# Optimization experiments

Hardware: AMD Instinct MI355X
Metric: run time of the kernel (lower is better)

## Reference

```python
import jax, jax.numpy as jnp
import numpy as np

B, T, C, NH = 4, 827, 1024, 16
HS = C // NH
SCALE = 1.0 / float(np.sqrt(HS))


def setup_inputs() -> dict:
    key = jax.random.key(0)
    ks = jax.random.split(key, 16)
    d = {}
    d["x"] = jax.random.normal(ks[0], (B, T, C), jnp.float32)
    d["x_kv"] = jax.random.normal(ks[1], (B, T, C), jnp.float32)
    d["h"] = jax.random.normal(ks[2], (B, NH, T, T), jnp.float32) * 0.1
    for i, name in enumerate(["f01", "f02", "f12", "b01", "b02", "b12"]):
        d[name] = jax.random.uniform(ks[3 + i], (B, 256, 256), jnp.float32)
    for i, name in enumerate(["Wq", "Wk", "Wv", "Wp"]):
        d[name] = jax.random.normal(ks[9 + i], (C, C), jnp.float32) * 0.02
    for name in ["bq", "bk", "bv", "bp"]:
        d[name] = jnp.zeros((C,), jnp.float32)
    return d


def _sm(a):
    return jax.nn.softmax(a, axis=-1)


def reference(x, x_kv, h, f01, f02, f12, b01, b02, b12,
              Wq, bq, Wk, bk, Wv, bv, Wp, bp):
    Bb, Tt, Cc = x.shape

    def heads(t):  # [B,T,C] -> [B,NH,T,HS]
        return t.reshape(Bb, Tt, NH, HS).transpose(0, 2, 1, 3)

    q = heads(x @ Wq.T + bq)
    k = heads(x_kv @ Wk.T + bk)
    v = heads(x_kv @ Wv.T + bv)

    att = jnp.einsum('bhqd,bhkd->bhqk', q, k) * SCALE + h  # adaptive bias add

    # region-specific partial softmax (frame1->frame0, frame2->frame0, frame2->frame1)
    att = att.at[:, :, 285:541, 0:256].set(_sm(att[:, :, 285:541, 0:256]))
    att = att.at[:, :, 571:827, 0:256].set(_sm(att[:, :, 571:827, 0:256]))
    att = att.at[:, :, 571:827, 286:542].set(_sm(att[:, :, 571:827, 286:542]))

    # bidirectional epipolar maps (backward maps used transposed)
    b01t = b01.transpose(0, 2, 1)
    b02t = b02.transpose(0, 2, 1)
    b12t = b12.transpose(0, 2, 1)
    m12 = (f12 * b12t >= 0.1).astype(att.dtype)  # [B,256,256]

    # bi_epi_ratio (T==827 branch), computed BEFORE the multiplicative masking
    r3 = att[:, :, 571:827, 286:542]            # [B,NH,256,256]
    att_mean = r3.mean(-1)                       # [B,NH,256]
    att_mask_mean = (r3 * m12[:, None]).sum(-1) / m12.sum(-1)[:, None]
    bi_epi_ratio = att_mask_mean.mean(1) / att_mean.mean(1)  # [B,256]

    # att_for: forward-only masking (clone); att: forward*backward masking
    att_for = att
    att_for = att_for.at[:, :, 285:541, 0:256].multiply(f01[:, None])
    att_for = att_for.at[:, :, 571:827, 0:256].multiply(f02[:, None])
    att_for = att_for.at[:, :, 571:827, 286:542].multiply(f12[:, None])
    att = att.at[:, :, 285:541, 0:256].multiply((b01t * f01)[:, None])
    att = att.at[:, :, 571:827, 0:256].multiply((b02t * f02)[:, None])
    att = att.at[:, :, 571:827, 286:542].multiply((b12t * f12)[:, None])

    causal = jnp.tril(jnp.ones((Tt, Tt), dtype=bool))
    aw = jnp.where(causal, att, -jnp.inf)
    # re-softmax of the already masked+multiplied regions (overwrites, then global softmax)
    aw = aw.at[:, :, 571:827, 0:256].set(_sm(att[:, :, 571:827, 0:256]))
    aw = aw.at[:, :, 571:827, 286:542].set(_sm(att[:, :, 571:827, 286:542]))
    aw = _sm(aw)

    y = jnp.einsum('bhqk,bhkd->bhqd', aw, v)
    y = y.transpose(0, 2, 1, 3).reshape(Bb, Tt, Cc)
    y = y @ Wp.T + bp  # resid dropout is identity (pdrop=0 / eval)
    return y, bi_epi_ratio
```

## Files before the change

### kernel.cpp

```cpp
#include <hip/hip_runtime.h>
#include <cstdint>
#include <cstddef>

#define Tn  827
#define Cn  1024
#define BTn 3308
#define TPn 832
#define YSZ 3387392

typedef unsigned short u16;
typedef unsigned short u16x4 __attribute__((ext_vector_type(4)));
typedef __bf16 bf16_t;
typedef bf16_t bf16x8 __attribute__((ext_vector_type(8)));
typedef float f32x4 __attribute__((ext_vector_type(4)));

__device__ inline u16 f32_to_bf16(float f) {
  union { float f; unsigned u; } v; v.f = f;
  unsigned u = v.u;
  u += 0x7fffu + ((u >> 16) & 1u);
  return (u16)(u >> 16);
}

__global__ __launch_bounds__(256)
void cvt_all_k(const float* __restrict__ x, const float* __restrict__ xkv,
               const float* __restrict__ wq, const float* __restrict__ wk,
               const float* __restrict__ wv, const float* __restrict__ wp,
               u16* __restrict__ xb, u16* __restrict__ xkb,
               u16* __restrict__ wqb, u16* __restrict__ wkb,
               u16* __restrict__ wvb, u16* __restrict__ wpb)
{
  const long NX = 846848;
  const long NW = 262144;
  long qidx = (long)blockIdx.x * 256 + threadIdx.x;
  const float* s; u16* d; long base;
  if (qidx < NX)            { s = x;   d = xb;  base = qidx; }
  else if (qidx < 2 * NX)   { s = xkv; d = xkb; base = qidx - NX; }
  else {
    long w = qidx - 2 * NX;
    int wi = (int)(w / NW);
    base = w - (long)wi * NW;
    if      (wi == 0) { s = wq; d = wqb; }
    else if (wi == 1) { s = wk; d = wkb; }
    else if (wi == 2) { s = wv; d = wvb; }
    else if (wi == 3) { s = wp; d = wpb; }
    else return;
  }
  const float4 v = *(const float4*)(s + base * 4);
  u16x4 o;
  o.x = f32_to_bf16(v.x); o.y = f32_to_bf16(v.y);
  o.z = f32_to_bf16(v.z); o.w = f32_to_bf16(v.w);
  *(u16x4*)(d + base * 4) = o;
}

template<int BM, int BN, int MODE>
__global__ __launch_bounds__(256)
void gemm_k(const u16* __restrict__ Aall, const u16* __restrict__ Ball,
            const float* __restrict__ bias, float* __restrict__ Cf,
            u16* __restrict__ Cb, int M, int N, int K, int lda, int ldb, int ldc)
{
  static_assert(BM == 128, "BM fixed at 128");
  constexpr int TM = BM / 32;
  constexpr int TN = BN / 32;

  const int tid  = threadIdx.x;
  const int lane = tid & 63;
  const int wave = tid >> 6;
  const int wm = wave >> 1, wn = wave & 1;
  const int m0 = blockIdx.x * BM;
  const int n0 = blockIdx.y * BN;

  __shared__ u16 As[BM * 32];
  __shared__ u16 Bs[BN * 32];

  f32x4 acc[TM][TN];
  const f32x4 zero4 = {0.f, 0.f, 0.f, 0.f};
  #pragma unroll
  for (int i = 0; i < TM; ++i)
    #pragma unroll
    for (int j = 0; j < TN; ++j)
      acc[i][j] = zero4;

  const int nk = K >> 5;

  for (int kt = 0; kt < nk; ++kt) {
    const int k0 = kt << 5;
    __syncthreads();
    #pragma unroll
    for (int it = 0; it < BM / 64; ++it) {
      const int cbase = it * 256 + wave * 64;
      const int c  = cbase + lane;
      const int r  = c >> 2;
      const int ko = (c & 3) << 3;
      if (m0 + r < M)
        __builtin_amdgcn_global_load_lds(
            (__attribute__((address_space(1))) void*)(Aall + (size_t)(m0 + r) * lda + k0 + ko),
            (__attribute__((address_space(3))) void*)(As + cbase * 8),
            16, 0, 0);
    }
    #pragma unroll
    for (int it = 0; it < BN / 64; ++it) {
      const int cbase = it * 256 + wave * 64;
      const int c  = cbase + lane;
      const int r  = c >> 2;
      const int ko = (c & 3) << 3;
      if (n0 + r < N)
        __builtin_amdgcn_global_load_lds(
            (__attribute__((address_space(1))) void*)(Ball + (size_t)(n0 + r) * ldb + k0 + ko),
            (__attribute__((address_space(3))) void*)(Bs + cbase * 8),
            16, 0, 0);
    }
    __syncthreads();

    bf16x8 af[TM], bfr[TN];
    #pragma unroll
    for (int i = 0; i < TM; ++i) {
      const int r = wm * 64 + i * 16 + (lane & 15);
      af[i] = *(const bf16x8*)(As + r * 32 + ((lane >> 4) << 3));
    }
    #pragma unroll
    for (int j = 0; j < TN; ++j) {
      const int r = wn * (TN * 16) + j * 16 + (lane & 15);
      bfr[j] = *(const bf16x8*)(Bs + r * 32 + ((lane >> 4) << 3));
    }
    #pragma unroll
    for (int i = 0; i < TM; ++i)
      #pragma unroll
      for (int j = 0; j < TN; ++j)
        acc[i][j] = __builtin_amdgcn_mfma_f32_16x16x32_bf16(af[i], bfr[j], acc[i][j], 0, 0, 0);
  }

  const int cq = lane >> 4, cl = lane & 15;
  #pragma unroll
  for (int i = 0; i < TM; ++i) {
    #pragma unroll
    for (int j = 0; j < TN; ++j) {
      const int rb  = m0 + wm * 64 + i * 16 + cq * 4;
      const int col = n0 + wn * (TN * 16) + j * 16 + cl;
      #pragma unroll
      for (int r = 0; r < 4; ++r) {
        const int row = rb + r;
        const float v = acc[i][j][r];
        if constexpr (MODE == 0) {
          if (row < M) Cb[(size_t)row * ldc + col] = f32_to_bf16(v + bias[col]);
        } else {
          if (row < M) Cf[(size_t)row * ldc + col] = v + bias[col];
        }
      }
    }
  }
}

__global__ __launch_bounds__(256)
void vtrans_k(const u16* __restrict__ V, u16* __restrict__ Vt)
{
  const int z = blockIdx.y;
  const int b = z >> 4, hh = z & 15;
  const int k0 = blockIdx.x * 64;
  const int tid = threadIdx.x;
  __shared__ u16 tile[64 * 65];
  #pragma unroll
  for (int rep = 0; rep < 16; ++rep) {
    const int idx = rep * 256 + tid;
    const int kl = idx >> 6, n = idx & 63;
    const int k = k0 + kl;
    u16 val = 0;
    if (k < Tn) val = V[((size_t)(b * Tn + k)) * Cn + hh * 64 + n];
    tile[n * 65 + kl] = val;
  }
  __syncthreads();
  #pragma unroll
  for (int rep = 0; rep < 16; ++rep) {
    const int idx = rep * 256 + tid;
    const int n = idx >> 6, kl = idx & 63;
    const int k = k0 + kl;
    if (k < TPn) Vt[((size_t)z * 64 + n) * TPn + k] = tile[n * 65 + kl];
  }
}

__global__ __launch_bounds__(256)
void btrans_k(const float* __restrict__ b01, const float* __restrict__ b02,
              const float* __restrict__ b12, float* __restrict__ bT)
{
  const int mb = blockIdx.z;
  const int rg = mb >> 2, bb = mb & 3;
  const float* src = (rg == 0 ? b01 : rg == 1 ? b02 : b12) + (size_t)bb * 65536;
  float* dst = bT + (size_t)mb * 65536;
  const int i0 = blockIdx.x * 64, j0 = blockIdx.y * 64;
  __shared__ float tile[64 * 65];
  const int tid = threadIdx.x;
  #pragma unroll
  for (int rep = 0; rep < 16; ++rep) {
    const int idx = rep * 256 + tid;
    const int jj = idx >> 6, ii = idx & 63;
    tile[ii * 65 + jj] = src[(size_t)(j0 + jj) * 256 + i0 + ii];
  }
  __syncthreads();
  #pragma unroll
  for (int rep = 0; rep < 16; ++rep) {
    const int idx = rep * 256 + tid;
    const int ii = idx >> 6, jj = idx & 63;
    dst[(size_t)(i0 + ii) * 256 + j0 + jj] = tile[ii * 65 + jj];
  }
}

__global__ __launch_bounds__(256)
void sreg_k(const u16* __restrict__ Qb, const u16* __restrict__ Kb,
            const float* __restrict__ hsrc, float* __restrict__ Sreg)
{
  const int zr = blockIdx.z;
  const int rg = zr % 3;
  const int z  = zr / 3;
  const int b = z >> 4, hh = z & 15;
  const int qoff = (rg == 0) ? 285 : 571;
  const int koff = (rg == 2) ? 286 : 0;
  const int m0 = blockIdx.x * 64;
  const int n0 = blockIdx.y * 64;

  const int tid = threadIdx.x;
  const int lane = tid & 63, wave = tid >> 6;
  const int quad = lane >> 4, cl = lane & 15;
  const int wm = wave >> 1, wn = wave & 1;

  __shared__ u16 As[2048], Bs[2048];

  const u16* Ab = Qb + ((size_t)(b * Tn + qoff + m0)) * Cn + hh * 64;
  const u16* Bb = Kb + ((size_t)(b * Tn + koff + n0)) * Cn + hh * 64;

  f32x4 acc[2][2];
  const f32x4 zero4 = {0.f, 0.f, 0.f, 0.f};
  acc[0][0] = zero4; acc[0][1] = zero4; acc[1][0] = zero4; acc[1][1] = zero4;

  #pragma unroll
  for (int kt = 0; kt < 2; ++kt) {
    const int k0 = kt * 32;
    __syncthreads();
    const int r = tid >> 2, ko = (tid & 3) << 3;
    __builtin_amdgcn_global_load_lds(
        (__attribute__((address_space(1))) void*)(Ab + (size_t)r * Cn + k0 + ko),
        (__attribute__((address_space(3))) void*)(&As[wave * 512]), 16, 0, 0);
    __builtin_amdgcn_global_load_lds(
        (__attribute__((address_space(1))) void*)(Bb + (size_t)r * Cn + k0 + ko),
        (__attribute__((address_space(3))) void*)(&Bs[wave * 512]), 16, 0, 0);
    __syncthreads();
    bf16x8 af[2], bfr[2];
    #pragma unroll
    for (int i = 0; i < 2; ++i)
      af[i] = *(const bf16x8*)(&As[(wm * 32 + i * 16 + cl) * 32 + quad * 8]);
    #pragma unroll
    for (int j = 0; j < 2; ++j)
      bfr[j] = *(const bf16x8*)(&Bs[(wn * 32 + j * 16 + cl) * 32 + quad * 8]);
    #pragma unroll
    for (int i = 0; i < 2; ++i)
      #pragma unroll
      for (int j = 0; j < 2; ++j)
        acc[i][j] = __builtin_amdgcn_mfma_f32_16x16x32_bf16(af[i], bfr[j], acc[i][j], 0, 0, 0);
  }

  float hvv[2][2][4];
  const size_t hb0 = (size_t)z * Tn * Tn;
  #pragma unroll
  for (int i = 0; i < 2; ++i)
    #pragma unroll
    for (int j = 0; j < 2; ++j)
      #pragma unroll
      for (int r = 0; r < 4; ++r) {
        const int row = m0 + wm * 32 + i * 16 + quad * 4 + r;
        const int col = n0 + wn * 32 + j * 16 + cl;
        hvv[i][j][r] = hsrc[hb0 + (size_t)(qoff + row) * Tn + koff + col];
      }
  float* outb = Sreg + ((size_t)zr << 16);
  #pragma unroll
  for (int i = 0; i < 2; ++i)
    #pragma unroll
    for (int j = 0; j < 2; ++j)
      #pragma unroll
      for (int r = 0; r < 4; ++r) {
        const int row = m0 + wm * 32 + i * 16 + quad * 4 + r;
        const int col = n0 + wn * 32 + j * 16 + cl;
        outb[(size_t)row * 256 + col] = acc[i][j][r] * 0.125f + hvv[i][j][r];
      }
}

__global__ __launch_bounds__(256)
void regional_k(float* __restrict__ Sreg, const float* __restrict__ f01,
                const float* __restrict__ f02, const float* __restrict__ f12,
                const float* __restrict__ bT,
                float* __restrict__ mmOut, float* __restrict__ amOut)
{
  const int tid  = threadIdx.x;
  const int lane = tid & 63;
  const int wrow = tid >> 6;
  const int row_id = blockIdx.x * 4 + wrow;
  const int region = row_id >> 14;
  const int rr = row_id & 16383;
  const int b  = rr >> 12;
  const int hh = (rr >> 8) & 15;
  const int i  = rr & 255;
  float* rp = Sreg + ((size_t)(((b * 16 + hh) * 3) + region) << 16) + (size_t)i * 256;

  const float* fp = (region == 0) ? f01 : (region == 1) ? f02 : f12;
  const float* bp = bT + ((size_t)(region * 4 + b) << 16);

  float v[4], fv[4], bv[4];
  #pragma unroll
  for (int t = 0; t < 4; ++t) {
    const int j = lane + 64 * t;
    v[t]  = rp[j];
    fv[t] = fp[((size_t)b * 256 + i) * 256 + j];
    bv[t] = bp[(size_t)i * 256 + j];
  }
  float mx = fmaxf(fmaxf(v[0], v[1]), fmaxf(v[2], v[3]));
  for (int m = 32; m > 0; m >>= 1) mx = fmaxf(mx, __shfl_xor(mx, m));
  float e[4], s = 0.f;
  #pragma unroll
  for (int t = 0; t < 4; ++t) { e[t] = __expf(v[t] - mx); s += e[t]; }
  for (int m = 32; m > 0; m >>= 1) s += __shfl_xor(s, m);
  const float inv = 1.f / s;
  float sm[4];
  #pragma unroll
  for (int t = 0; t < 4; ++t) sm[t] = e[t] * inv;

  if (region == 2) {
    float msum = 0.f, mcnt = 0.f, asum = 0.f;
    #pragma unroll
    for (int t = 0; t < 4; ++t) {
      const float mk = (fv[t] * bv[t] >= 0.1f) ? 1.f : 0.f;
      msum += sm[t] * mk; mcnt += mk; asum += sm[t];
    }
    for (int m = 32; m > 0; m >>= 1) {
      msum += __shfl_xor(msum, m);
      mcnt += __shfl_xor(mcnt, m);
      asum += __shfl_xor(asum, m);
    }
    if (lane == 0) {
      const int idx = (b * 16 + hh) * 256 + i;
      mmOut[idx] = msum / mcnt;
      amOut[idx] = asum * (1.f / 256.f);
    }
  }

  float mult[4];
  #pragma unroll
  for (int t = 0; t < 4; ++t) mult[t] = sm[t] * fv[t] * bv[t];

  if (region == 0) {
    #pragma unroll
    for (int t = 0; t < 4; ++t) rp[lane + 64 * t] = mult[t];
  } else {
    float mx2 = fmaxf(fmaxf(mult[0], mult[1]), fmaxf(mult[2], mult[3]));
    for (int m = 32; m > 0; m >>= 1) mx2 = fmaxf(mx2, __shfl_xor(mx2, m));
    float e2[4], s2 = 0.f;
    #pragma unroll
    for (int t = 0; t < 4; ++t) { e2[t] = __expf(mult[t] - mx2); s2 += e2[t]; }
    for (int m = 32; m > 0; m >>= 1) s2 += __shfl_xor(s2, m);
    const float inv2 = 1.f / s2;
    #pragma unroll
    for (int t = 0; t < 4; ++t) rp[lane + 64 * t] = e2[t] * inv2;
  }
}

__global__ __launch_bounds__(256)
void flash_k(const u16* __restrict__ Qb, const u16* __restrict__ Kb,
             const u16* __restrict__ Vt, const float* __restrict__ hsrc,
             const float* __restrict__ Sreg, u16* __restrict__ ya)
{
  const int bid = blockIdx.x;
  const int zlow = bid & 7;
  const int t = bid >> 3;
  const int qt = t % 13;
  const int zhigh = t / 13;
  const int z = zhigh * 8 + zlow;
  const int b = z >> 4, hh = z & 15;
  const int q0 = qt * 64;

  const int tid = threadIdx.x;
  const int lane = tid & 63;
  const int wave = tid >> 6;
  const int quad = lane >> 4;
  const int cl = lane & 15;

  __shared__ u16 Qs[2][2048];
  __shared__ u16 Ks[2][2048];
  __shared__ u16 Vs[2][2048];
  __shared__ u16 Ps[4][2][512];

  {
    const u16* src = Qb + ((size_t)(b * Tn + q0)) * Cn + hh * 64;
    const int r = tid >> 2;
    const int ko = (tid & 3) << 3;
    #pragma unroll
    for (int p = 0; p < 2; ++p)
      __builtin_amdgcn_global_load_lds(
          (__attribute__((address_space(1))) void*)(src + (size_t)r * Cn + p * 32 + ko),
          (__attribute__((address_space(3))) void*)(&Qs[p][wave * 512]), 16, 0, 0);
  }
  __syncthreads();

  bf16x8 qa[2];
  #pragma unroll
  for (int p = 0; p < 2; ++p)
    qa[p] = *(const bf16x8*)(&Qs[p][(wave * 16 + cl) * 32 + quad * 8]);

  f32x4 Oa[4];
  const f32x4 zero4 = {0.f, 0.f, 0.f, 0.f};
  Oa[0] = zero4; Oa[1] = zero4; Oa[2] = zero4; Oa[3] = zero4;
  float mrow[4] = {-3.0e38f, -3.0e38f, -3.0e38f, -3.0e38f};
  float lrow[4] = {0.f, 0.f, 0.f, 0.f};

  const size_t hbase = (size_t)z * Tn * Tn;
  const int qrow_base = q0 + wave * 16 + quad * 4;

  for (int kt = 0; kt <= qt; ++kt) {
    const int k0 = kt * 64;
    __syncthreads();
    {
      const u16* ksrc = Kb + ((size_t)(b * Tn + k0)) * Cn + hh * 64;
      const u16* vsrc = Vt + ((size_t)(z * 64)) * TPn + k0;
      const int r = tid >> 2;
      const int ko = (tid & 3) << 3;
      #pragma unroll
      for (int p = 0; p < 2; ++p) {
        __builtin_amdgcn_global_load_lds(
            (__attribute__((address_space(1))) void*)(ksrc + (size_t)r * Cn + p * 32 + ko),
            (__attribute__((address_space(3))) void*)(&Ks[p][wave * 512]), 16, 0, 0);
        __builtin_amdgcn_global_load_lds(
            (__attribute__((address_space(1))) void*)(vsrc + (size_t)r * TPn + p * 32 + ko),
            (__attribute__((address_space(3))) void*)(&Vs[p][wave * 512]), 16, 0, 0);
      }
    }
    float hv[4][4];
    unsigned rmask = 0;
    #pragma unroll
    for (int j = 0; j < 4; ++j) {
      const int kk = k0 + j * 16 + cl;
      #pragma unroll
      for (int r = 0; r < 4; ++r) {
        const int qq = qrow_base + r;
        const float* p = hsrc + hbase + (size_t)qq * Tn + kk;
        bool isreg = false;
        if (kk < 542) {
          if (qq >= 571 && qq < Tn) {
            if (kk < 256) {
              p = Sreg + (((size_t)(z * 3 + 1)) << 16) + (size_t)(qq - 571) * 256 + kk;
              isreg = true;
            } else if (kk >= 286) {
              p = Sreg + (((size_t)(z * 3 + 2)) << 16) + (size_t)(qq - 571) * 256 + (kk - 286);
              isreg = true;
            }
          } else if (qq >= 285 && qq < 541 && kk < 256) {
            p = Sreg + (((size_t)(z * 3 + 0)) << 16) + (size_t)(qq - 285) * 256 + kk;
            isreg = true;
          }
        }
        const bool valid = (kk <= qq) && (qq < Tn);
        hv[j][r] = valid ? *p : 0.f;
        if (isreg) rmask |= 1u << (j * 4 + r);
      }
    }
    __syncthreads();

    f32x4 sa[4];
    sa[0] = zero4; sa[1] = zero4; sa[2] = zero4; sa[3] = zero4;
    #pragma unroll
    for (int p = 0; p < 2; ++p) {
      #pragma unroll
      for (int n = 0; n < 4; ++n) {
        const bf16x8 kb = *(const bf16x8*)(&Ks[p][(n * 16 + cl) * 32 + quad * 8]);
        sa[n] = __builtin_amdgcn_mfma_f32_16x16x32_bf16(qa[p], kb, sa[n], 0, 0, 0);
      }
    }

    #pragma unroll
    for (int r = 0; r < 4; ++r) {
      const int qq = qrow_base + r;
      float sv[4];
      #pragma unroll
      for (int j = 0; j < 4; ++j) {
        const int kk = k0 + j * 16 + cl;
        const float vv = ((rmask >> (j * 4 + r)) & 1)
                             ? hv[j][r]
                             : sa[j][r] * 0.125f + hv[j][r];
        sv[j] = (kk <= qq && qq < Tn) ? vv : -3.0e38f;
      }
      float mx = fmaxf(fmaxf(sv[0], sv[1]), fmaxf(sv[2], sv[3]));
      mx = fmaxf(mx, __shfl_xor(mx, 1));
      mx = fmaxf(mx, __shfl_xor(mx, 2));
      mx = fmaxf(mx, __shfl_xor(mx, 4));
      mx = fmaxf(mx, __shfl_xor(mx, 8));
      const float mnew = fmaxf(mrow[r], mx);
      const float alpha = __expf(mrow[r] - mnew);
      mrow[r] = mnew;
      float ps[4], psum = 0.f;
      #pragma unroll
      for (int j = 0; j < 4; ++j) { ps[j] = __expf(sv[j] - mnew); psum += ps[j]; }
      psum += __shfl_xor(psum, 1);
      psum += __shfl_xor(psum, 2);
      psum += __shfl_xor(psum, 4);
      psum += __shfl_xor(psum, 8);
      lrow[r] = lrow[r] * alpha + psum;
      #pragma unroll
      for (int n = 0; n < 4; ++n) Oa[n][r] *= alpha;
      #pragma unroll
      for (int j = 0; j < 4; ++j)
        Ps[wave][j >> 1][(quad * 4 + r) * 32 + (j & 1) * 16 + cl] = f32_to_bf16(ps[j]);
    }

    #pragma unroll
    for (int p = 0; p < 2; ++p) {
      const bf16x8 pa = *(const bf16x8*)(&Ps[wave][p][cl * 32 + quad * 8]);
      #pragma unroll
      for (int n = 0; n < 4; ++n) {
        const bf16x8 vb = *(const bf16x8*)(&Vs[p][(n * 16 + cl) * 32 + quad * 8]);
        Oa[n] = __builtin_amdgcn_mfma_f32_16x16x32_bf16(pa, vb, Oa[n], 0, 0, 0);
      }
    }
  }

  #pragma unroll
  for (int r = 0; r < 4; ++r) {
    const int qq = qrow_base + r;
    if (qq >= Tn) continue;
    const float inv = 1.f / lrow[r];
    u16* op = ya + ((size_t)(b * Tn + qq)) * Cn + hh * 64;
    #pragma unroll
    for (int n = 0; n < 4; ++n)
      op[n * 16 + cl] = f32_to_bf16(Oa[n][r] * inv);
  }
}

__global__ __launch_bounds__(256)
void ratio_k(const float* __restrict__ mm, const float* __restrict__ am,
             float* __restrict__ out)
{
  const int idx = blockIdx.x * 256 + threadIdx.x;
  const int b = idx >> 8, i = idx & 255;
  float smm = 0.f, sam = 0.f;
  #pragma unroll
  for (int hh = 0; hh < 16; ++hh) {
    smm += mm[(b * 16 + hh) * 256 + i];
    sam += am[(b * 16 + hh) * 256 + i];
  }
  out[idx] = smm / sam;
}

extern "C" void kernel_launch(void* const* d_in, const int* in_sizes, int n_in,
                              void* d_out, int out_size, void* d_ws, size_t ws_size,
                              hipStream_t stream)
{
  (void)in_sizes; (void)n_in; (void)out_size;

  const float* x   = (const float*)d_in[0];
  const float* xkv = (const float*)d_in[1];
  const float* hb  = (const float*)d_in[2];
  const float* f01 = (const float*)d_in[3];
  const float* f02 = (const float*)d_in[4];
  const float* f12 = (const float*)d_in[5];
  const float* b01 = (const float*)d_in[6];
  const float* b02 = (const float*)d_in[7];
  const float* b12 = (const float*)d_in[8];
  const float* Wq  = (const float*)d_in[9];
  const float* Wk  = (const float*)d_in[10];
  const float* Wv  = (const float*)d_in[11];
  const float* Wp  = (const float*)d_in[12];
  const float* bq  = (const float*)d_in[13];
  const float* bk  = (const float*)d_in[14];
  const float* bv  = (const float*)d_in[15];
  const float* bp  = (const float*)d_in[16];
  float* out = (float*)d_out;

  char* ws = (char*)d_ws;
  u16* xb   = (u16*)(ws + 0);
  u16* xkb  = (u16*)(ws + 6774784);
  u16* wqb  = (u16*)(ws + 13549568);
  u16* wkb  = (u16*)(ws + 15646720);
  u16* wvb  = (u16*)(ws + 17743872);
  u16* wpb  = (u16*)(ws + 19841024);
  u16* Qb   = (u16*)(ws + 21938176);
  u16* Kb   = (u16*)(ws + 28712960);
  u16* Vb   = (u16*)(ws + 35487744);
  u16* Vt   = (u16*)(ws + 42262528);
  u16* ya   = (u16*)(ws + 49078272);
  float* Sreg = (float*)(ws + 55853056);
  float* bT = (float*)(ws + 106184704);
  float* mm = (float*)(ws + 109330432);
  float* am = (float*)(ws + 109395968);
  const size_t need = 109461504;
  if (ws_size < need) return;

  cvt_all_k<<<dim3(10712), 256, 0, stream>>>(x, xkv, Wq, Wk, Wv, Wp,
                                             xb, xkb, wqb, wkb, wvb, wpb);
  btrans_k<<<dim3(4, 4, 12), 256, 0, stream>>>(b01, b02, b12, bT);
  gemm_k<128,64,0><<<dim3(26,16,1),256,0,stream>>>(xb,  wqb, bq, nullptr, Qb, BTn, Cn, Cn, Cn, Cn, Cn);
  gemm_k<128,64,0><<<dim3(26,16,1),256,0,stream>>>(xkb, wkb, bk, nullptr, Kb, BTn, Cn, Cn, Cn, Cn, Cn);
  gemm_k<128,64,0><<<dim3(26,16,1),256,0,stream>>>(xkb, wvb, bv, nullptr, Vb, BTn, Cn, Cn, Cn, Cn, Cn);
  vtrans_k<<<dim3(13,64),256,0,stream>>>(Vb, Vt);
  sreg_k<<<dim3(4,4,192),256,0,stream>>>(Qb, Kb, hb, Sreg);
  regional_k<<<dim3(12288),256,0,stream>>>(Sreg, f01, f02, f12, bT, mm, am);
  flash_k<<<dim3(832),256,0,stream>>>(Qb, Kb, Vt, hb, Sreg, ya);
  gemm_k<128,64,3><<<dim3(26,16,1),256,0,stream>>>(ya, wpb, bp, out, nullptr, BTn, Cn, Cn, Cn, Cn, Cn);
  ratio_k<<<dim3(4),256,0,stream>>>(mm, am, out + YSZ);
}
```

Measured before the change: 472.8 us.

## Rewrite projection GEMMs with register-staged double buffering and fused K/V launch

```diff
diff --git a/kernel.cpp b/kernel.cpp
--- a/kernel.cpp
+++ b/kernel.cpp
@@ -52,98 +52,106 @@
   *(u16x4*)(d + base * 4) = o;
 }
 
-template<int BM, int BN, int MODE>
-__global__ __launch_bounds__(256)
-void gemm_k(const u16* __restrict__ Aall, const u16* __restrict__ Ball,
-            const float* __restrict__ bias, float* __restrict__ Cf,
-            u16* __restrict__ Cb, int M, int N, int K, int lda, int ldb, int ldc)
-{
-  static_assert(BM == 128, "BM fixed at 128");
-  constexpr int TM = BM / 32;
-  constexpr int TN = BN / 32;
+template<int MODE>
+__global__ __launch_bounds__(256)
+void pgemm_k(const u16* __restrict__ A, const u16* __restrict__ Bw,
+             const float* __restrict__ bias, const float* __restrict__ bias2,
+             float* __restrict__ Cf, u16* __restrict__ Cb, u16* __restrict__ Cb2,
+             int M, int N)
+{
+  constexpr int BM = 128, BN = 64, BK = 64, STB = 144;
+  __shared__ u16 As[2][BM * 72];
+  __shared__ u16 Bs[2][BN * 72];
 
   const int tid  = threadIdx.x;
   const int lane = tid & 63;
   const int wave = tid >> 6;
+  const int quad = lane >> 4, cl = lane & 15;
   const int wm = wave >> 1, wn = wave & 1;
   const int m0 = blockIdx.x * BM;
   const int n0 = blockIdx.y * BN;
 
-  __shared__ u16 As[BM * 32];
-  __shared__ u16 Bs[BN * 32];
-
-  f32x4 acc[TM][TN];
+  float4 av[4], bv[2];
+
+  auto loadT = [&](int kt) {
+    const int k0 = kt * BK;
+    #pragma unroll
+    for (int i = 0; i < 4; ++i) {
+      const int c = tid + 256 * i;
+      int gr = m0 + (c >> 3);
+      if (gr >= M) gr = M - 1;
+      av[i] = *(const float4*)(A + (size_t)gr * 1024 + k0 + (c & 7) * 8);
+    }
+    #pragma unroll
+    for (int i = 0; i < 2; ++i) {
+      const int c = tid + 256 * i;
+      bv[i] = *(const float4*)(Bw + (size_t)(n0 + (c >> 3)) * 1024 + k0 + (c & 7) * 8);
+    }
+  };
+  auto writeT = [&](int nb) {
+    #pragma unroll
+    for (int i = 0; i < 4; ++i) {
+      const int c = tid + 256 * i;
+      *(float4*)((char*)&As[nb][0] + (c >> 3) * STB + (c & 7) * 16) = av[i];
+    }
+    #pragma unroll
+    for (int i = 0; i < 2; ++i) {
+      const int c = tid + 256 * i;
+      *(float4*)((char*)&Bs[nb][0] + (c >> 3) * STB + (c & 7) * 16) = bv[i];
+    }
+  };
+
+  f32x4 acc[4][2];
   const f32x4 zero4 = {0.f, 0.f, 0.f, 0.f};
   #pragma unroll
-  for (int i = 0; i < TM; ++i)
-    #pragma unroll
-    for (int j = 0; j < TN; ++j)
-      acc[i][j] = zero4;
-
-  const int nk = K >> 5;
-
-  for (int kt = 0; kt < nk; ++kt) {
-    const int k0 = kt << 5;
+  for (int i = 0; i < 4; ++i) { acc[i][0] = zero4; acc[i][1] = zero4; }
+
+  loadT(0);
+  writeT(0);
+  __syncthreads();
+
+  for (int kt = 0; kt < 16; ++kt) {
+    const int cur = kt & 1;
+    if (kt < 15) loadT(kt + 1);
+    #pragma unroll
+    for (int ks = 0; ks < 2; ++ks) {
+      bf16x8 af[4], bfr[2];
+      #pragma unroll
+      for (int i = 0; i < 4; ++i)
+        af[i] = *(const bf16x8*)((const char*)&As[cur][0] +
+                                 (wm * 64 + i * 16 + cl) * STB + ks * 64 + quad * 16);
+      #pragma unroll
+      for (int j = 0; j < 2; ++j)
+        bfr[j] = *(const bf16x8*)((const char*)&Bs[cur][0] +
+                                  (wn * 32 + j * 16 + cl) * STB + ks * 64 + quad * 16);
+      #pragma unroll
+      for (int i = 0; i < 4; ++i)
+        #pragma unroll
+        for (int j = 0; j < 2; ++j)
+          acc[i][j] = __builtin_amdgcn_mfma_f32_16x16x32_bf16(af[i], bfr[j], acc[i][j], 0, 0, 0);
+    }
+    if (kt < 15) writeT(cur ^ 1);
     __syncthreads();
-    #pragma unroll
-    for (int it = 0; it < BM / 64; ++it) {
-      const int cbase = it * 256 + wave * 64;
-      const int c  = cbase + lane;
-      const int r  = c >> 2;
-      const int ko = (c & 3) << 3;
-      if (m0 + r < M)
-        __builtin_amdgcn_global_load_lds(
-            (__attribute__((address_space(1))) void*)(Aall + (size_t)(m0 + r) * lda + k0 + ko),
-            (__attribute__((address_space(3))) void*)(As + cbase * 8),
-            16, 0, 0);
-    }
-    #pragma unroll
-    for (int it = 0; it < BN / 64; ++it) {
-      const int cbase = it * 256 + wave * 64;
-      const int c  = cbase + lane;
-      const int r  = c >> 2;
-      const int ko = (c & 3) << 3;
-      if (n0 + r < N)
-        __builtin_amdgcn_global_load_lds(
-            (__attribute__((address_space(1))) void*)(Ball + (size_t)(n0 + r) * ldb + k0 + ko),
-            (__attribute__((address_space(3))) void*)(Bs + cbase * 8),
-            16, 0, 0);
-    }
-    __syncthreads();
-
-    bf16x8 af[TM], bfr[TN];
-    #pragma unroll
-    for (int i = 0; i < TM; ++i) {
-      const int r = wm * 64 + i * 16 + (lane & 15);
-      af[i] = *(const bf16x8*)(As + r * 32 + ((lane >> 4) << 3));
-    }
-    #pragma unroll
-    for (int j = 0; j < TN; ++j) {
-      const int r = wn * (TN * 16) + j * 16 + (lane & 15);
-      bfr[j] = *(const bf16x8*)(Bs + r * 32 + ((lane >> 4) << 3));
-    }
-    #pragma unroll
-    for (int i = 0; i < TM; ++i)
-      #pragma unroll
-      for (int j = 0; j < TN; ++j)
-        acc[i][j] = __builtin_amdgcn_mfma_f32_16x16x32_bf16(af[i], bfr[j], acc[i][j], 0, 0, 0);
-  }
-
-  const int cq = lane >> 4, cl = lane & 15;
-  #pragma unroll
-  for (int i = 0; i < TM; ++i) {
-    #pragma unroll
-    for (int j = 0; j < TN; ++j) {
-      const int rb  = m0 + wm * 64 + i * 16 + cq * 4;
-      const int col = n0 + wn * (TN * 16) + j * 16 + cl;
+  }
+
+  #pragma unroll
+  for (int i = 0; i < 4; ++i) {
+    #pragma unroll
+    for (int j = 0; j < 2; ++j) {
+      const int rb  = m0 + wm * 64 + i * 16 + quad * 4;
+      const int col = n0 + wn * 32 + j * 16 + cl;
       #pragma unroll
       for (int r = 0; r < 4; ++r) {
         const int row = rb + r;
+        if (row >= M) continue;
         const float v = acc[i][j][r];
         if constexpr (MODE == 0) {
-          if (row < M) Cb[(size_t)row * ldc + col] = f32_to_bf16(v + bias[col]);
+          Cb[(size_t)row * 1024 + col] = f32_to_bf16(v + bias[col]);
+        } else if constexpr (MODE == 4) {
+          if (col < 1024) Cb[(size_t)row * 1024 + col] = f32_to_bf16(v + bias[col]);
+          else            Cb2[(size_t)row * 1024 + col - 1024] = f32_to_bf16(v + bias2[col - 1024]);
         } else {
-          if (row < M) Cf[(size_t)row * ldc + col] = v + bias[col];
+          Cf[(size_t)row * 1024 + col] = v + bias[col];
         }
       }
     }
@@ -590,13 +598,12 @@
   cvt_all_k<<<dim3(10712), 256, 0, stream>>>(x, xkv, Wq, Wk, Wv, Wp,
                                              xb, xkb, wqb, wkb, wvb, wpb);
   btrans_k<<<dim3(4, 4, 12), 256, 0, stream>>>(b01, b02, b12, bT);
-  gemm_k<128,64,0><<<dim3(26,16,1),256,0,stream>>>(xb,  wqb, bq, nullptr, Qb, BTn, Cn, Cn, Cn, Cn, Cn);
-  gemm_k<128,64,0><<<dim3(26,16,1),256,0,stream>>>(xkb, wkb, bk, nullptr, Kb, BTn, Cn, Cn, Cn, Cn, Cn);
-  gemm_k<128,64,0><<<dim3(26,16,1),256,0,stream>>>(xkb, wvb, bv, nullptr, Vb, BTn, Cn, Cn, Cn, Cn, Cn);
+  pgemm_k<0><<<dim3(26,16),256,0,stream>>>(xb,  wqb, bq, nullptr, nullptr, Qb, nullptr, BTn, 1024);
+  pgemm_k<4><<<dim3(26,32),256,0,stream>>>(xkb, wkb, bk, bv, nullptr, Kb, Vb, BTn, 2048);
   vtrans_k<<<dim3(13,64),256,0,stream>>>(Vb, Vt);
   sreg_k<<<dim3(4,4,192),256,0,stream>>>(Qb, Kb, hb, Sreg);
   regional_k<<<dim3(12288),256,0,stream>>>(Sreg, f01, f02, f12, bT, mm, am);
   flash_k<<<dim3(832),256,0,stream>>>(Qb, Kb, Vt, hb, Sreg, ya);
-  gemm_k<128,64,3><<<dim3(26,16,1),256,0,stream>>>(ya, wpb, bp, out, nullptr, BTn, Cn, Cn, Cn, Cn, Cn);
+  pgemm_k<3><<<dim3(26,16),256,0,stream>>>(ya, wpb, bp, nullptr, out, nullptr, nullptr, BTn, 1024);
   ratio_k<<<dim3(4),256,0,stream>>>(mm, am, out + YSZ);
 }
```

New measurement: 540.6 us. +14.4%, slower.
